# Optimization experiments

Measured on AMD Instinct MI355X. Metric: run time of the kernel, lower is better.

The kernel has to match this reference:

```python
import jax, jax.numpy as jnp
import numpy as np

B, S, D, H = 64, 512, 544, 1024  # batch, seq, state_dim+pb_dim, n_hid


def setup_inputs() -> dict:
    key = jax.random.key(0)
    k_x, k_wih, k_whh, k_bih, k_bhh = jax.random.split(key, 5)
    bound = 1.0 / np.sqrt(H)  # PyTorch LSTM uniform init range
    X = jax.random.normal(k_x, (B, S, D), dtype=jnp.float32)
    W_ih = jax.random.uniform(k_wih, (4 * H, D), jnp.float32, -bound, bound)
    W_hh = jax.random.uniform(k_whh, (4 * H, H), jnp.float32, -bound, bound)
    b_ih = jax.random.uniform(k_bih, (4 * H,), jnp.float32, -bound, bound)
    b_hh = jax.random.uniform(k_bhh, (4 * H,), jnp.float32, -bound, bound)
    return {"X": X, "W_ih": W_ih, "W_hh": W_hh, "b_ih": b_ih, "b_hh": b_hh}


def reference(X, W_ih, W_hh, b_ih, b_hh):
    # Faithful to PBRNN.forward: LSTM scanned over the sequence dim
    # (the torch code loops one timestep at a time; the math is a plain
    # single-layer LSTM from zero initial state). Returns final (h, c)
    # stacked as [2, B, H] — the only state forward() produces.
    n_batch = X.shape[0]
    n_hid = W_hh.shape[1]
    Xs = jnp.swapaxes(X, 0, 1)  # [S, B, D]
    # Precompute input projections for all timesteps: [S, B, 4H]
    x_proj = jnp.einsum('sbd,gd->sbg', Xs, W_ih) + (b_ih + b_hh)

    def step(carry, xp):
        h, c = carry
        gates = xp + h @ W_hh.T  # [B, 4H]
        i, f, g, o = jnp.split(gates, 4, axis=-1)  # PyTorch gate order i,f,g,o
        i = jax.nn.sigmoid(i)
        f = jax.nn.sigmoid(f)
        g = jnp.tanh(g)
        o = jax.nn.sigmoid(o)
        c = f * c + i * g
        h = o * jnp.tanh(c)
        return (h, c), None

    h0 = jnp.zeros((n_batch, n_hid), dtype=X.dtype)
    c0 = jnp.zeros((n_batch, n_hid), dtype=X.dtype)
    (h_n, c_n), _ = jax.lax.scan(step, (h0, c0), x_proj)
    return jnp.stack([h_n, c_n])  # [2, B, H]
```

## Files before the change

kernel.cpp:

```cpp
#include <hip/hip_runtime.h>
#include <hip/hip_bf16.h>


#define B_  64
#define S_  512
#define D_  544
#define H_  1024
#define CG_ 64
#define BG_ 4
#define GRID_ (CG_*BG_)

typedef __attribute__((ext_vector_type(8))) short bf16x8;
typedef __attribute__((ext_vector_type(4))) float f32x4;

__device__ inline ushort f2b(float x){
  unsigned u = __float_as_uint(x);
  u = (u + 0x7FFFu + ((u >> 16) & 1u)) >> 16;
  return (ushort)u;
}

__device__ inline bf16x8 pack8(float4 a, float4 b){
  bf16x8 r;
  r[0]=(short)f2b(a.x); r[1]=(short)f2b(a.y); r[2]=(short)f2b(a.z); r[3]=(short)f2b(a.w);
  r[4]=(short)f2b(b.x); r[5]=(short)f2b(b.y); r[6]=(short)f2b(b.z); r[7]=(short)f2b(b.w);
  return r;
}

__device__ inline unsigned long long ld64a(const unsigned long long* q){
  return __hip_atomic_load(q, __ATOMIC_RELAXED, __HIP_MEMORY_SCOPE_AGENT);
}

__device__ inline float sigm(float x){ return __builtin_amdgcn_rcpf(1.f + __expf(-x)); }
__device__ inline float tanh_(float x){ return 1.f - 2.f*__builtin_amdgcn_rcpf(1.f + __expf(2.f*x)); }

__global__ void cvt_x(const float* __restrict__ x, ushort* __restrict__ xb, int n4){
  int i = blockIdx.x*256 + threadIdx.x;
  if (i >= n4) return;
  float4 v = ((const float4*)x)[i];
  ushort4 o;
  o.x=f2b(v.x); o.y=f2b(v.y); o.z=f2b(v.z); o.w=f2b(v.w);
  ((ushort4*)xb)[i] = o;
}

__global__ __launch_bounds__(256,1) void lstm_persist(
    const float* __restrict__ Wih, const float* __restrict__ Whh,
    const float* __restrict__ bih, const float* __restrict__ bhh,
    const ushort* __restrict__ Xb,
    unsigned* thbuf,
    float* __restrict__ out)
{
  const int tid  = threadIdx.x;
  const int wave = tid >> 6;
  const int lane = tid & 63;
  const int c16  = lane & 15;
  const int quad = lane >> 4;
  const int bg   = (blockIdx.x & 7) >> 1;
  const int cg   = ((blockIdx.x >> 3) << 1) | (blockIdx.x & 1);

  __shared__ float gates_s[2][4][64][17];

  bf16x8 whhf[4][8];
  #pragma unroll
  for (int mt = 0; mt < 4; ++mt){
    const size_t grow = (size_t)(mt*H_ + cg*16 + c16);
    #pragma unroll
    for (int i = 0; i < 8; ++i){
      int k = wave*256 + i*32 + quad*8;
      const float4* p = (const float4*)(Whh + grow*H_ + k);
      whhf[mt][i] = pack8(p[0], p[1]);
    }
  }
  bf16x8 wihf[4][5];
  #pragma unroll
  for (int mt = 0; mt < 4; ++mt){
    const size_t grow = (size_t)(mt*H_ + cg*16 + c16);
    #pragma unroll
    for (int ii = 0; ii < 5; ++ii){
      int it = wave + 4*ii;
      if (it < 17){
        int k = it*32 + quad*8;
        const float4* p = (const float4*)(Wih + grow*D_ + k);
        wihf[mt][ii] = pack8(p[0], p[1]);
      }
    }
  }

  const int uu = tid & 15;
  const int nn = tid >> 4;
  float bsum[4];
  #pragma unroll
  for (int g = 0; g < 4; ++g)
    bsum[g] = bih[g*H_ + cg*16 + uu] + bhh[g*H_ + cg*16 + uu];
  float cstate = 0.f;

  f32x4 acc[4];
  bf16x8 xraw[5];

  auto zacc = [&]{
    #pragma unroll
    for (int mt = 0; mt < 4; ++mt) acc[mt] = (f32x4){0.f,0.f,0.f,0.f};
  };
  auto ldx = [&](int t){
    if (t >= S_) t = S_-1;
    #pragma unroll
    for (int ii = 0; ii < 5; ++ii){
      int it = wave + 4*ii;
      if (it < 17)
        xraw[ii] = *(const bf16x8*)(Xb + ((size_t)(bg*16 + c16)*S_ + t)*D_ + it*32 + quad*8);
    }
  };
  auto xp_mfma = [&]{
    #pragma unroll
    for (int ii = 0; ii < 5; ++ii){
      int it = wave + 4*ii;
      if (it < 17){
        #pragma unroll
        for (int mt = 0; mt < 4; ++mt)
          acc[mt] = __builtin_amdgcn_mfma_f32_16x16x32_bf16(wihf[mt][ii], xraw[ii], acc[mt], 0,0,0);
      }
    }
  };

  ldx(0);
  zacc();
  xp_mfma();
  ldx(1);

  const int obase = (bg*64 + wave*16 + (quad>>1))*256 + c16*16 + (quad&1)*8;

  for (int t = 0; t < S_; ++t){
    const unsigned* hp = thbuf + (t & 1) * (B_*H_);
    unsigned*       hn = thbuf + ((t & 1) ^ 1) * (B_*H_);

    unsigned long long q[8][4];
    {
      const unsigned tag = (unsigned)t & 0xffffu;
      const unsigned long long tmask = 0xffff0000ffff0000ull;
      const unsigned long long texp  = ((unsigned long long)tag << 16)
                                     | ((unsigned long long)tag << 48);
      const unsigned long long* pb[8];
      #pragma unroll
      for (int i = 0; i < 8; ++i){
        pb[i] = (const unsigned long long*)(hp + obase + i*512);
        q[i][0] = ld64a(pb[i]);   q[i][1] = ld64a(pb[i]+1);
        q[i][2] = ld64a(pb[i]+2); q[i][3] = ld64a(pb[i]+3);
      }
      unsigned stale = 0xffu;
      long rounds = 0;
      while (stale){
        unsigned ns = 0;
        #pragma unroll
        for (int i = 0; i < 8; ++i){
          if (stale & (1u << i)){
            unsigned long long d = ((q[i][0]^texp)|(q[i][1]^texp)
                                   |(q[i][2]^texp)|(q[i][3]^texp)) & tmask;
            if (d != 0ull){
              q[i][0] = ld64a(pb[i]);   q[i][1] = ld64a(pb[i]+1);
              q[i][2] = ld64a(pb[i]+2); q[i][3] = ld64a(pb[i]+3);
              ns |= (1u << i);
            }
          }
        }
        stale = ns;
        if (++rounds > (1L<<20)) break;
      }
    }
    #pragma unroll
    for (int i = 0; i < 8; ++i){
      union { unsigned u[4]; bf16x8 v8; } eb;
      #pragma unroll
      for (int w = 0; w < 4; ++w){
        unsigned lo = (unsigned)q[i][w];
        unsigned hi = (unsigned)(q[i][w] >> 32);
        eb.u[w] = (lo & 0xffffu) | (hi << 16);
      }
      #pragma unroll
      for (int mt = 0; mt < 4; ++mt)
        acc[mt] = __builtin_amdgcn_mfma_f32_16x16x32_bf16(whhf[mt][i], eb.v8, acc[mt], 0,0,0);
    }

    #pragma unroll
    for (int mt = 0; mt < 4; ++mt)
      #pragma unroll
      for (int r = 0; r < 4; ++r)
        gates_s[t & 1][wave][mt*16 + quad*4 + r][c16] = acc[mt][r];
    __syncthreads();

    {
      float gsum[4];
      #pragma unroll
      for (int g = 0; g < 4; ++g){
        float s = bsum[g];
        #pragma unroll
        for (int q2 = 0; q2 < 4; ++q2) s += gates_s[t & 1][q2][g*16 + uu][nn];
        gsum[g] = s;
      }
      float iv = sigm(gsum[0]), fv = sigm(gsum[1]), gv = tanh_(gsum[2]), ov = sigm(gsum[3]);
      float cn = fv*cstate + iv*gv;
      cstate = cn;
      float hv = ov*tanh_(cn);
      unsigned word = (((unsigned)(t+1) & 0xffffu) << 16) | (unsigned)f2b(hv);
      __hip_atomic_store(hn + (size_t)(bg*64 + cg)*256 + tid, word,
                         __ATOMIC_RELAXED, __HIP_MEMORY_SCOPE_AGENT);
      if (t == S_-1){
        out[(bg*16 + nn)*H_ + cg*16 + uu]          = hv;
        out[B_*H_ + (bg*16 + nn)*H_ + cg*16 + uu]  = cn;
      }
    }

    if (t < S_-1){
      zacc();
      xp_mfma();
      ldx(t + 2);
    }
  }
}

extern "C" void kernel_launch(void* const* d_in, const int* in_sizes, int n_in,
                              void* d_out, int out_size, void* d_ws, size_t ws_size,
                              hipStream_t stream) {
  const float* X   = (const float*)d_in[0];
  const float* Wih = (const float*)d_in[1];
  const float* Whh = (const float*)d_in[2];
  const float* bih = (const float*)d_in[3];
  const float* bhh = (const float*)d_in[4];
  float* out = (float*)d_out;

  char* ws = (char*)d_ws;
  const size_t THBUF_BYTES = 2ull * B_ * H_ * sizeof(unsigned);
  const size_t XB_OFF      = THBUF_BYTES;
  const size_t XB_BYTES    = (size_t)B_ * S_ * D_ * sizeof(ushort);
  if (ws_size < XB_OFF + XB_BYTES) return;

  unsigned* thbuf = (unsigned*)ws;
  ushort*   Xb    = (ushort*)(ws + XB_OFF);

  hipMemsetAsync(d_ws, 0, THBUF_BYTES, stream);

  int n4 = B_*S_*D_/4;
  cvt_x<<<(n4 + 255)/256, 256, 0, stream>>>(X, Xb, n4);
  lstm_persist<<<GRID_, 256, 0, stream>>>(Wih, Whh, bih, bhh, Xb, thbuf, out);
}
```

Before: 2.343 ms.

## Halve grid to 128 blocks of 512 threads with LDS-staged h exchange

Restructures the persistent LSTM kernel to 128 workgroups of 512 threads, each owning 32 hidden columns for 16 batch rows. The previous hidden state is polled from global memory cooperatively and staged into swizzled LDS instead of each wave polling its own fragment. Gate partial sums are now reduced with LDS atomics. The aim is to cut the number of cross-block participants in the per-step barrier-like handshake and the amount of redundant global polling. In exchange it adds an extra __syncthreads, LDS atomic contention, and more register pressure per block under launch_bounds(512,2).

```diff
diff --git a/kernel.cpp b/kernel.cpp
--- a/kernel.cpp
+++ b/kernel.cpp
@@ -1,17 +1,18 @@
 #include <hip/hip_runtime.h>
-#include <hip/hip_bf16.h>
 
 
 #define B_  64
 #define S_  512
 #define D_  544
 #define H_  1024
-#define CG_ 64
+#define NCG 32
 #define BG_ 4
-#define GRID_ (CG_*BG_)
+#define GRID_ (NCG*BG_)
+#define THR_ 512
 
 typedef __attribute__((ext_vector_type(8))) short bf16x8;
 typedef __attribute__((ext_vector_type(4))) float f32x4;
+typedef unsigned long long u64;
 
 __device__ inline ushort f2b(float x){
   unsigned u = __float_as_uint(x);
@@ -26,7 +27,7 @@
   return r;
 }
 
-__device__ inline unsigned long long ld64a(const unsigned long long* q){
+__device__ inline u64 ld64a(const u64* q){
   return __hip_atomic_load(q, __ATOMIC_RELAXED, __HIP_MEMORY_SCOPE_AGENT);
 }
 
@@ -42,7 +43,7 @@
   ((ushort4*)xb)[i] = o;
 }
 
-__global__ __launch_bounds__(256,1) void lstm_persist(
+__global__ __launch_bounds__(THR_,2) void lstm_persist(
     const float* __restrict__ Wih, const float* __restrict__ Whh,
     const float* __restrict__ bih, const float* __restrict__ bhh,
     const ushort* __restrict__ Xb,
@@ -54,164 +55,186 @@
   const int lane = tid & 63;
   const int c16  = lane & 15;
   const int quad = lane >> 4;
-  const int bg   = (blockIdx.x & 7) >> 1;
-  const int cg   = ((blockIdx.x >> 3) << 1) | (blockIdx.x & 1);
-
-  __shared__ float gates_s[2][4][64][17];
-
-  bf16x8 whhf[4][8];
-  #pragma unroll
-  for (int mt = 0; mt < 4; ++mt){
-    const size_t grow = (size_t)(mt*H_ + cg*16 + c16);
-    #pragma unroll
-    for (int i = 0; i < 8; ++i){
-      int k = wave*256 + i*32 + quad*8;
-      const float4* p = (const float4*)(Whh + grow*H_ + k);
-      whhf[mt][i] = pack8(p[0], p[1]);
-    }
-  }
-  bf16x8 wihf[4][5];
-  #pragma unroll
-  for (int mt = 0; mt < 4; ++mt){
-    const size_t grow = (size_t)(mt*H_ + cg*16 + c16);
-    #pragma unroll
-    for (int ii = 0; ii < 5; ++ii){
-      int it = wave + 4*ii;
-      if (it < 17){
-        int k = it*32 + quad*8;
+  const int kq   = wave >> 1;
+  const int gh   = wave & 1;
+
+  const int bg = (blockIdx.x & 7) >> 1;
+  const int cg = ((blockIdx.x >> 3) << 1) | (blockIdx.x & 1);
+
+  __shared__ __align__(16) char h_s[16*1024*2];
+  __shared__ float gsum[4][32][17];
+
+  bf16x8 whhf[2][2][8];
+  #pragma unroll
+  for (int g2 = 0; g2 < 2; ++g2){
+    #pragma unroll
+    for (int cb = 0; cb < 2; ++cb){
+      const size_t grow = (size_t)((gh*2+g2)*H_ + cg*32 + cb*16 + c16);
+      #pragma unroll
+      for (int i = 0; i < 8; ++i){
+        int k = kq*256 + i*32 + quad*8;
+        const float4* p = (const float4*)(Whh + grow*H_ + k);
+        whhf[g2][cb][i] = pack8(p[0], p[1]);
+      }
+    }
+  }
+  bf16x8 wihf[2][2][4];
+  #pragma unroll
+  for (int g2 = 0; g2 < 2; ++g2){
+    #pragma unroll
+    for (int cb = 0; cb < 2; ++cb){
+      const size_t grow = (size_t)((gh*2+g2)*H_ + cg*32 + cb*16 + c16);
+      #pragma unroll
+      for (int ii = 0; ii < 4; ++ii){
+        int k = (kq + 4*ii)*32 + quad*8;
         const float4* p = (const float4*)(Wih + grow*D_ + k);
-        wihf[mt][ii] = pack8(p[0], p[1]);
-      }
-    }
-  }
-
-  const int uu = tid & 15;
-  const int nn = tid >> 4;
+        wihf[g2][cb][ii] = pack8(p[0], p[1]);
+      }
+    }
+  }
+  bf16x8 wihf16;
+  {
+    const size_t grow = (size_t)((gh*2 + (kq>>1))*H_ + cg*32 + (kq&1)*16 + c16);
+    const float4* p = (const float4*)(Wih + grow*D_ + 512 + quad*8);
+    wihf16 = pack8(p[0], p[1]);
+  }
+
+  const int ucol = tid & 31;
+  const int ub   = tid >> 5;
   float bsum[4];
   #pragma unroll
   for (int g = 0; g < 4; ++g)
-    bsum[g] = bih[g*H_ + cg*16 + uu] + bhh[g*H_ + cg*16 + uu];
+    bsum[g] = bih[g*H_ + cg*32 + ucol] + bhh[g*H_ + cg*32 + ucol];
   float cstate = 0.f;
 
-  f32x4 acc[4];
-  bf16x8 xraw[5];
+  #pragma unroll
+  for (int g = 0; g < 4; ++g) gsum[g][ucol][ub] = 0.f;
+
+  f32x4 acc[2][2];
+  bf16x8 xraw[4]; bf16x8 xraw16;
 
   auto zacc = [&]{
     #pragma unroll
-    for (int mt = 0; mt < 4; ++mt) acc[mt] = (f32x4){0.f,0.f,0.f,0.f};
+    for (int g2 = 0; g2 < 2; ++g2)
+      #pragma unroll
+      for (int cb = 0; cb < 2; ++cb) acc[g2][cb] = (f32x4){0.f,0.f,0.f,0.f};
   };
   auto ldx = [&](int t){
-    if (t >= S_) t = S_-1;
-    #pragma unroll
-    for (int ii = 0; ii < 5; ++ii){
-      int it = wave + 4*ii;
-      if (it < 17)
-        xraw[ii] = *(const bf16x8*)(Xb + ((size_t)(bg*16 + c16)*S_ + t)*D_ + it*32 + quad*8);
-    }
+    const ushort* xrow = Xb + ((size_t)(bg*16 + c16)*S_ + t)*D_;
+    #pragma unroll
+    for (int ii = 0; ii < 4; ++ii)
+      xraw[ii] = *(const bf16x8*)(xrow + (kq + 4*ii)*32 + quad*8);
+    xraw16 = *(const bf16x8*)(xrow + 512 + quad*8);
   };
   auto xp_mfma = [&]{
     #pragma unroll
-    for (int ii = 0; ii < 5; ++ii){
-      int it = wave + 4*ii;
-      if (it < 17){
-        #pragma unroll
-        for (int mt = 0; mt < 4; ++mt)
-          acc[mt] = __builtin_amdgcn_mfma_f32_16x16x32_bf16(wihf[mt][ii], xraw[ii], acc[mt], 0,0,0);
-      }
-    }
+    for (int ii = 0; ii < 4; ++ii)
+      #pragma unroll
+      for (int g2 = 0; g2 < 2; ++g2)
+        #pragma unroll
+        for (int cb = 0; cb < 2; ++cb)
+          acc[g2][cb] = __builtin_amdgcn_mfma_f32_16x16x32_bf16(wihf[g2][cb][ii], xraw[ii], acc[g2][cb], 0,0,0);
+    if      (kq==0) acc[0][0] = __builtin_amdgcn_mfma_f32_16x16x32_bf16(wihf16, xraw16, acc[0][0], 0,0,0);
+    else if (kq==1) acc[0][1] = __builtin_amdgcn_mfma_f32_16x16x32_bf16(wihf16, xraw16, acc[0][1], 0,0,0);
+    else if (kq==2) acc[1][0] = __builtin_amdgcn_mfma_f32_16x16x32_bf16(wihf16, xraw16, acc[1][0], 0,0,0);
+    else            acc[1][1] = __builtin_amdgcn_mfma_f32_16x16x32_bf16(wihf16, xraw16, acc[1][1], 0,0,0);
   };
 
   ldx(0);
   zacc();
   xp_mfma();
-  ldx(1);
-
-  const int obase = (bg*64 + wave*16 + (quad>>1))*256 + c16*16 + (quad&1)*8;
 
   for (int t = 0; t < S_; ++t){
     const unsigned* hp = thbuf + (t & 1) * (B_*H_);
     unsigned*       hn = thbuf + ((t & 1) ^ 1) * (B_*H_);
-
-    unsigned long long q[8][4];
-    {
-      const unsigned tag = (unsigned)t & 0xffffu;
-      const unsigned long long tmask = 0xffff0000ffff0000ull;
-      const unsigned long long texp  = ((unsigned long long)tag << 16)
-                                     | ((unsigned long long)tag << 48);
-      const unsigned long long* pb[8];
-      #pragma unroll
-      for (int i = 0; i < 8; ++i){
-        pb[i] = (const unsigned long long*)(hp + obase + i*512);
-        q[i][0] = ld64a(pb[i]);   q[i][1] = ld64a(pb[i]+1);
-        q[i][2] = ld64a(pb[i]+2); q[i][3] = ld64a(pb[i]+3);
-      }
-      unsigned stale = 0xffu;
-      long rounds = 0;
+    const unsigned tag = (unsigned)t & 0xffffu;
+    const u64 tmask = 0xffff0000ffff0000ull;
+    const u64 texp  = ((u64)tag << 16) | ((u64)tag << 48);
+
+    #pragma unroll
+    for (int pair = 0; pair < 2; ++pair){
+      u64 q[2][4];
+      const u64* pb[2];
+      #pragma unroll
+      for (int f = 0; f < 2; ++f){
+        int F = (pair*2 + f)*THR_ + tid;
+        pb[f] = (const u64*)(hp + bg*16384 + F*8);
+        q[f][0]=ld64a(pb[f]);   q[f][1]=ld64a(pb[f]+1);
+        q[f][2]=ld64a(pb[f]+2); q[f][3]=ld64a(pb[f]+3);
+      }
+      unsigned stale = 3u;
+      int rounds = 0;
       while (stale){
         unsigned ns = 0;
         #pragma unroll
-        for (int i = 0; i < 8; ++i){
-          if (stale & (1u << i)){
-            unsigned long long d = ((q[i][0]^texp)|(q[i][1]^texp)
-                                   |(q[i][2]^texp)|(q[i][3]^texp)) & tmask;
+        for (int f = 0; f < 2; ++f){
+          if (stale & (1u<<f)){
+            u64 d = ((q[f][0]^texp)|(q[f][1]^texp)|(q[f][2]^texp)|(q[f][3]^texp)) & tmask;
             if (d != 0ull){
-              q[i][0] = ld64a(pb[i]);   q[i][1] = ld64a(pb[i]+1);
-              q[i][2] = ld64a(pb[i]+2); q[i][3] = ld64a(pb[i]+3);
-              ns |= (1u << i);
+              q[f][0]=ld64a(pb[f]);   q[f][1]=ld64a(pb[f]+1);
+              q[f][2]=ld64a(pb[f]+2); q[f][3]=ld64a(pb[f]+3);
+              ns |= (1u<<f);
             }
           }
         }
         stale = ns;
-        if (++rounds > (1L<<20)) break;
-      }
-    }
+        if (++rounds > (1<<20)) break;
+      }
+      #pragma unroll
+      for (int f = 0; f < 2; ++f){
+        int F  = (pair*2 + f)*THR_ + tid;
+        int b  = (F >> 1) & 15;
+        int k0 = (F >> 5)*16 + (F & 1)*8;
+        uint4 pv;
+        pv.x = (unsigned)(q[f][0] & 0xffffu) | (unsigned)((q[f][0] >> 16) & 0xffff0000u);
+        pv.y = (unsigned)(q[f][1] & 0xffffu) | (unsigned)((q[f][1] >> 16) & 0xffff0000u);
+        pv.z = (unsigned)(q[f][2] & 0xffffu) | (unsigned)((q[f][2] >> 16) & 0xffff0000u);
+        pv.w = (unsigned)(q[f][3] & 0xffffu) | (unsigned)((q[f][3] >> 16) & 0xffff0000u);
+        int byte = (b*2048 + k0*2) ^ ((b & 7) << 4);
+        *(uint4*)(h_s + byte) = pv;
+      }
+    }
+    __syncthreads();
+
     #pragma unroll
     for (int i = 0; i < 8; ++i){
-      union { unsigned u[4]; bf16x8 v8; } eb;
-      #pragma unroll
-      for (int w = 0; w < 4; ++w){
-        unsigned lo = (unsigned)q[i][w];
-        unsigned hi = (unsigned)(q[i][w] >> 32);
-        eb.u[w] = (lo & 0xffffu) | (hi << 16);
-      }
-      #pragma unroll
-      for (int mt = 0; mt < 4; ++mt)
-        acc[mt] = __builtin_amdgcn_mfma_f32_16x16x32_bf16(whhf[mt][i], eb.v8, acc[mt], 0,0,0);
-    }
-
-    #pragma unroll
-    for (int mt = 0; mt < 4; ++mt)
-      #pragma unroll
-      for (int r = 0; r < 4; ++r)
-        gates_s[t & 1][wave][mt*16 + quad*4 + r][c16] = acc[mt][r];
+      int byte = (c16*2048 + kq*512 + i*64 + quad*16) ^ ((c16 & 7) << 4);
+      bf16x8 hb = *(const bf16x8*)(h_s + byte);
+      #pragma unroll
+      for (int g2 = 0; g2 < 2; ++g2)
+        #pragma unroll
+        for (int cb = 0; cb < 2; ++cb)
+          acc[g2][cb] = __builtin_amdgcn_mfma_f32_16x16x32_bf16(whhf[g2][cb][i], hb, acc[g2][cb], 0,0,0);
+    }
+    #pragma unroll
+    for (int g2 = 0; g2 < 2; ++g2)
+      #pragma unroll
+      for (int cb = 0; cb < 2; ++cb)
+        #pragma unroll
+        for (int r = 0; r < 4; ++r)
+          atomicAdd(&gsum[gh*2+g2][cb*16 + quad*4 + r][c16], acc[g2][cb][r]);
     __syncthreads();
 
-    {
-      float gsum[4];
-      #pragma unroll
-      for (int g = 0; g < 4; ++g){
-        float s = bsum[g];
-        #pragma unroll
-        for (int q2 = 0; q2 < 4; ++q2) s += gates_s[t & 1][q2][g*16 + uu][nn];
-        gsum[g] = s;
-      }
-      float iv = sigm(gsum[0]), fv = sigm(gsum[1]), gv = tanh_(gsum[2]), ov = sigm(gsum[3]);
-      float cn = fv*cstate + iv*gv;
-      cstate = cn;
-      float hv = ov*tanh_(cn);
-      unsigned word = (((unsigned)(t+1) & 0xffffu) << 16) | (unsigned)f2b(hv);
-      __hip_atomic_store(hn + (size_t)(bg*64 + cg)*256 + tid, word,
-                         __ATOMIC_RELAXED, __HIP_MEMORY_SCOPE_AGENT);
-      if (t == S_-1){
-        out[(bg*16 + nn)*H_ + cg*16 + uu]          = hv;
-        out[B_*H_ + (bg*16 + nn)*H_ + cg*16 + uu]  = cn;
-      }
-    }
-
-    if (t < S_-1){
+    if (t < S_-1) ldx(t+1);
+    float gs[4];
+    #pragma unroll
+    for (int g = 0; g < 4; ++g) gs[g] = bsum[g] + gsum[g][ucol][ub];
+    #pragma unroll
+    for (int g = 0; g < 4; ++g) gsum[g][ucol][ub] = 0.f;
+    float iv = sigm(gs[0]), fv = sigm(gs[1]), gv = tanh_(gs[2]), ov = sigm(gs[3]);
+    float cn = fv*cstate + iv*gv;
+    cstate = cn;
+    float hv = ov*tanh_(cn);
+    unsigned word = (((unsigned)(t+1) & 0xffffu) << 16) | (unsigned)f2b(hv);
+    int colg = cg*32 + ucol;
+    __hip_atomic_store(hn + bg*16384 + (colg >> 4)*256 + ub*16 + (colg & 15), word,
+                       __ATOMIC_RELAXED, __HIP_MEMORY_SCOPE_AGENT);
+    if (t == S_-1){
+      out[(bg*16 + ub)*H_ + colg]          = hv;
+      out[B_*H_ + (bg*16 + ub)*H_ + colg]  = cn;
+    } else {
       zacc();
       xp_mfma();
-      ldx(t + 2);
     }
   }
 }
@@ -239,5 +262,5 @@
 
   int n4 = B_*S_*D_/4;
   cvt_x<<<(n4 + 255)/256, 256, 0, stream>>>(X, Xb, n4);
-  lstm_persist<<<GRID_, 256, 0, stream>>>(Wih, Whh, bih, bhh, Xb, thbuf, out);
-}
+  lstm_persist<<<GRID_, THR_, 0, stream>>>(Wih, Whh, bih, bhh, Xb, thbuf, out);
+}
```

Measured after the change: 9.151 ms. +290.5%, slower.
